# Kernel optimization log

Hardware: AMD Instinct MI355X
Metric: run time of the kernel (lower is better)

Reference implementation:

```python
import jax, jax.numpy as jnp
import numpy as np

N_NODES = 40000
N_EDGES = 640000
D_IN = 128
D_OUT = 128


def setup_inputs() -> dict:
    key = jax.random.key(0)
    k1, k2, k3 = jax.random.split(key, 3)
    x = jax.random.normal(k1, (N_NODES, D_IN), dtype=jnp.float32)
    W = jax.random.normal(k2, (D_IN, D_OUT), dtype=jnp.float32) / np.sqrt(D_IN)
    b = jnp.zeros((D_OUT,), dtype=jnp.float32)
    edge_index = jax.random.randint(k3, (2, N_EDGES), 0, N_NODES, dtype=jnp.int64)
    return {"x": x, "W": W, "b": b, "edge_index": edge_index}


def reference(x, W, b, edge_index):
    src, dst = edge_index[0], edge_index[1]
    n = x.shape[0]
    # asymmetric normalization: 1 / out-degree(src), inf -> 0
    deg = jax.ops.segment_sum(jnp.ones_like(src, dtype=x.dtype), src, num_segments=n)
    deg_inv = jnp.where(deg > 0, 1.0 / deg, 0.0)
    # GCNConv (add_self_loops=False, normalize=False): h = x @ W; msg_e = w_e * h[src_e]
    h = x @ W  # [N, D_OUT]
    msg = h[src] * deg_inv[src][:, None]  # [E, D_OUT] gather-weighted messages
    out = jax.ops.segment_sum(msg, dst, num_segments=n) + b  # scatter-add to dst
    return out
```

## Files before the change

kernel.cpp:

```cpp
#include <hip/hip_runtime.h>

#define N_NODES 40000
#define D 128
#define N_EDGES 640000
#define GRP 128
#define NKEY 313
#define TSIZE 2048
#define NTILE 313
#define GCAP 2560
#define NSLICE 32
#define SLICE_E 20000
#define SLICE_E4 5000
#define HALF_BINS 20000
#define HALF_W 10000
#define WROW 20000
#define SRCH_BLKS 64
#define GEMM_BLKS 625
#define XP 136

typedef __attribute__((ext_vector_type(8))) short short8_t;
typedef __attribute__((ext_vector_type(4))) float float4_t;

static __device__ __forceinline__ unsigned short f2bf(float f) {
  unsigned u = __float_as_uint(f);
  return (unsigned short)((u + 0x7fffu + ((u >> 16) & 1u)) >> 16);
}
static __device__ __forceinline__ float bf2f(unsigned short h) {
  return __uint_as_float(((unsigned)h) << 16);
}

static __device__ __forceinline__ void scan512(unsigned* s, int tid) {
  const int t2 = tid + 256;
#pragma unroll
  for (int off = 1; off < 512; off <<= 1) {
    unsigned a = (tid >= off) ? s[tid - off] : 0u;
    unsigned c = (t2 >= off) ? s[t2 - off] : 0u;
    __syncthreads();
    s[tid] += a;
    s[t2] += c;
    __syncthreads();
  }
}

__global__ __launch_bounds__(256) void k1(
    const float* __restrict__ x, const float* __restrict__ W,
    const int* __restrict__ src, const int* __restrict__ dst,
    unsigned* __restrict__ slabS, unsigned* __restrict__ slabP,
    unsigned* __restrict__ lofs, unsigned* __restrict__ epackT,
    unsigned short* __restrict__ hb) {
  __shared__ unsigned smem[12544];
  const int bid = blockIdx.x;
  const int tid = threadIdx.x;

  if (bid < SRCH_BLKS) {
    const int b = bid >> 1;
    const int h = bid & 1;
    for (int i = tid; i < HALF_W; i += 256) smem[i] = 0;
    __syncthreads();
    const int4* p4 = (const int4*)(src + b * SLICE_E);
    const unsigned lo = (unsigned)(h * HALF_BINS);
    for (int it = tid; it < SLICE_E4; it += 256) {
      const int4 v = p4[it];
      unsigned u;
      u = (unsigned)v.x - lo; if (u < HALF_BINS) atomicAdd(&smem[u >> 1], 1u << ((u & 1) * 16));
      u = (unsigned)v.y - lo; if (u < HALF_BINS) atomicAdd(&smem[u >> 1], 1u << ((u & 1) * 16));
      u = (unsigned)v.z - lo; if (u < HALF_BINS) atomicAdd(&smem[u >> 1], 1u << ((u & 1) * 16));
      u = (unsigned)v.w - lo; if (u < HALF_BINS) atomicAdd(&smem[u >> 1], 1u << ((u & 1) * 16));
    }
    __syncthreads();
    unsigned* row = slabS + (size_t)b * WROW + h * HALF_W;
    for (int i = tid; i < HALF_W; i += 256) row[i] = smem[i];
    return;
  }

  const int t = bid - SRCH_BLKS;
  if (t % 3 == 2) {
    const int cid = t / 3;
    unsigned* cnt = smem;
    unsigned* cur = smem + 320;
    unsigned* s = smem + 640;
    unsigned* buf = smem + 1152;
    const int t2 = tid + 256;
    if (tid < NKEY) cnt[tid] = 0;
    if (t2 < NKEY) cnt[t2] = 0;
    __syncthreads();

    const int e0 = cid * TSIZE;
    const int nE = (N_EDGES - e0) < TSIZE ? (N_EDGES - e0) : TSIZE;
    int4 sa, sb, da, db;
    const bool act = (tid * 8) < nE;
    if (act) {
      sa = *(const int4*)(src + e0 + tid * 8);
      sb = *(const int4*)(src + e0 + tid * 8 + 4);
      da = *(const int4*)(dst + e0 + tid * 8);
      db = *(const int4*)(dst + e0 + tid * 8 + 4);
      atomicAdd(&cnt[da.x >> 7], 1u);
      atomicAdd(&cnt[da.y >> 7], 1u);
      atomicAdd(&cnt[da.z >> 7], 1u);
      atomicAdd(&cnt[da.w >> 7], 1u);
      atomicAdd(&cnt[db.x >> 7], 1u);
      atomicAdd(&cnt[db.y >> 7], 1u);
      atomicAdd(&cnt[db.z >> 7], 1u);
      atomicAdd(&cnt[db.w >> 7], 1u);
    }
    __syncthreads();

    const unsigned v0 = (tid < NKEY) ? cnt[tid] : 0u;
    const unsigned v1 = (t2 < NKEY) ? cnt[t2] : 0u;
    s[tid] = v0;
    s[t2] = v1;
    __syncthreads();
    scan512(s, tid);
    if (tid < NKEY) {
      const unsigned ex = s[tid] - v0;
      cur[tid] = ex;
      slabP[(size_t)cid * NKEY + tid] = v0;
      lofs[(size_t)cid * NKEY + tid] = ex;
    }
    if (t2 < NKEY) {
      const unsigned ex = s[t2] - v1;
      cur[t2] = ex;
      slabP[(size_t)cid * NKEY + t2] = v1;
      lofs[(size_t)cid * NKEY + t2] = ex;
    }
    __syncthreads();

    if (act) {
#define TPLACE(DV, SV)                                                \
  {                                                                   \
    const int d_ = (DV);                                              \
    const unsigned r_ = atomicAdd(&cur[d_ >> 7], 1u);                 \
    buf[r_] = ((unsigned)(d_ & 127) << 16) | (unsigned)(SV);          \
  }
      TPLACE(da.x, sa.x) TPLACE(da.y, sa.y) TPLACE(da.z, sa.z) TPLACE(da.w, sa.w)
      TPLACE(db.x, sb.x) TPLACE(db.y, sb.y) TPLACE(db.z, sb.z) TPLACE(db.w, sb.w)
#undef TPLACE
    }
    __syncthreads();
    for (int i = tid; i < nE; i += 256) epackT[e0 + i] = buf[i];
    return;
  }

  const int gid = 2 * (t / 3) + (t % 3);
  if (gid >= GEMM_BLKS) return;
  const int n0 = gid * 64;
  const int w = tid >> 6;
  const int lane = tid & 63;

  unsigned short* wb = (unsigned short*)smem;
  unsigned short* xb = wb + 16384;

#pragma unroll 4
  for (int i = 0; i < 16; ++i) {
    const int g4 = i * 256 + tid;
    const int k = g4 >> 5;
    const int d0 = (g4 & 31) * 4;
    const float4 v = ((const float4*)W)[g4];
    const int q = k >> 5, r = k & 31;
    const int base =
        (((d0 >> 4) * 4 + q) * 64 + ((r >> 3) * 16 + (d0 & 15))) * 8 + (r & 7);
    wb[base] = f2bf(v.x);
    wb[base + 8] = f2bf(v.y);
    wb[base + 16] = f2bf(v.z);
    wb[base + 24] = f2bf(v.w);
  }

  {
    const float4* xg = (const float4*)(x + (size_t)n0 * D);
#pragma unroll
    for (int j = 0; j < 8; ++j) {
      const int idx = tid + j * 256;
      const int row = idx >> 5;
      const int c4 = idx & 31;
      const float4 v = xg[idx];
      ushort4 o;
      o.x = f2bf(v.x); o.y = f2bf(v.y); o.z = f2bf(v.z); o.w = f2bf(v.w);
      *(ushort4*)(xb + row * XP + c4 * 4) = o;
    }
  }
  __syncthreads();

  short8_t afrag[4];
  {
    const unsigned short* ap0 = xb + (w * 16 + (lane & 15)) * XP + (lane >> 4) * 8;
#pragma unroll
    for (int q = 0; q < 4; ++q) afrag[q] = *(const short8_t*)(ap0 + q * 32);
  }

  const int orow = n0 + w * 16 + (lane >> 4) * 4;
  const int ocolbase = lane & 15;
#pragma unroll
  for (int t8 = 0; t8 < 8; ++t8) {
    float4_t acc = {0.f, 0.f, 0.f, 0.f};
#pragma unroll
    for (int q = 0; q < 4; ++q) {
      const short8_t bfrag = *(const short8_t*)(wb + ((t8 * 4 + q) * 64 + lane) * 8);
      acc = __builtin_amdgcn_mfma_f32_16x16x32_bf16(afrag[q], bfrag, acc, 0, 0, 0);
    }
    const int col = t8 * 16 + ocolbase;
#pragma unroll
    for (int r = 0; r < 4; ++r)
      hb[(size_t)(orow + r) * D + col] = f2bf(acc[r]);
  }
}

__global__ __launch_bounds__(256) void k4a(
    const unsigned* __restrict__ slabP, const unsigned* __restrict__ lofs,
    const unsigned* __restrict__ epackT, const unsigned* __restrict__ slabS,
    int* __restrict__ offs, int* __restrict__ cnt_dst,
    unsigned short* __restrict__ esrc16, float* __restrict__ dinv) {
  const int bid = blockIdx.x;
  const int tid = threadIdx.x;

  if (bid < NKEY) {
    const int k = bid;
    __shared__ unsigned chb[NTILE];
    __shared__ unsigned chc[NTILE];
    __shared__ unsigned cnt[GRP];
    __shared__ unsigned cur[GRP];
    __shared__ unsigned s[256];

    for (int t = tid; t < NTILE; t += 256) {
      chc[t] = slabP[(size_t)t * NKEY + k];
      chb[t] = t * TSIZE + lofs[(size_t)t * NKEY + k];
    }
    if (tid < GRP) cnt[tid] = 0;
    __syncthreads();

    for (int t = tid; t < NTILE; t += 256) {
      const unsigned base = chb[t];
      const unsigned c = chc[t];
      for (unsigned e = 0; e < c; ++e) {
        atomicAdd(&cnt[epackT[base + e] >> 16], 1u);
      }
    }
    __syncthreads();

    const unsigned v = (tid < GRP) ? cnt[tid] : 0u;
    s[tid] = v;
    __syncthreads();
#pragma unroll
    for (int off = 1; off < 256; off <<= 1) {
      unsigned a = (tid >= off) ? s[tid - off] : 0u;
      __syncthreads();
      s[tid] += a;
      __syncthreads();
    }
    if (tid < GRP) {
      const unsigned ex = s[tid] - v;
      cur[tid] = ex;
      const int n = k * GRP + tid;
      if (n < N_NODES) {
        offs[n] = (int)(k * GCAP + ex);
        cnt_dst[n] = (int)v;
      }
    }
    __syncthreads();

    for (int t = tid; t < NTILE; t += 256) {
      const unsigned base = chb[t];
      const unsigned c = chc[t];
      for (unsigned e = 0; e < c; ++e) {
        const unsigned p = epackT[base + e];
        const unsigned r = atomicAdd(&cur[p >> 16], 1u);
        if (r < GCAP) esrc16[(size_t)k * GCAP + r] = (unsigned short)(p & 0xFFFFu);
      }
    }
    return;
  }

  const int w = (bid - NKEY) * 256 + tid;
  if (w >= WROW) return;
  unsigned run = 0;
#pragma unroll 8
  for (int b = 0; b < NSLICE; ++b) run += slabS[(size_t)b * WROW + w];
  const unsigned lo = run & 0xFFFFu;
  const unsigned hi = run >> 16;
  dinv[2 * w] = lo ? 1.0f / (float)lo : 0.0f;
  dinv[2 * w + 1] = hi ? 1.0f / (float)hi : 0.0f;
}

__global__ __launch_bounds__(256) void k4b(
    const int* __restrict__ offs, const int* __restrict__ cnt_dst,
    const float* __restrict__ dinv, const unsigned short* __restrict__ esrc16,
    const unsigned short* __restrict__ hb,
    const float* __restrict__ b, float* __restrict__ out) {
  const int tid = threadIdx.x;
  const int node = blockIdx.x * 8 + (tid >> 5);
  const int lane = tid & 31;

  const int start = offs[node];
  const int len = cnt_dst[node];
  const unsigned short* bk = esrc16 + start;

  int sj = 0;
  if (lane < len) sj = bk[lane];
  const float fj = dinv[sj];

  float4 aa[4];
#pragma unroll
  for (int q = 0; q < 4; ++q) aa[q] = make_float4(0.f, 0.f, 0.f, 0.f);

  const int l32 = len < 32 ? len : 32;
  for (int jj = 0; jj < l32; jj += 8) {
    ushort4 u[8];
    float fq[8];
#pragma unroll
    for (int q = 0; q < 8; ++q) {
      const int j = jj + q;
      const int s = __shfl(sj, j, 32);
      const float f = __shfl(fj, j, 32);
      const bool on = j < l32;
      const int ss = on ? s : 0;
      u[q] = ((const ushort4*)(hb + (size_t)ss * D))[lane];
      fq[q] = on ? f : 0.0f;
    }
#pragma unroll
    for (int q = 0; q < 8; ++q) {
      const float f = fq[q];
      float4& a = aa[q & 3];
      a.x += f * bf2f(u[q].x);
      a.y += f * bf2f(u[q].y);
      a.z += f * bf2f(u[q].z);
      a.w += f * bf2f(u[q].w);
    }
  }
  for (int j = 32; j < len; ++j) {
    const int s = bk[j];
    const float f = dinv[s];
    ushort4 u = ((const ushort4*)(hb + (size_t)s * D))[lane];
    aa[0].x += f * bf2f(u.x);
    aa[0].y += f * bf2f(u.y);
    aa[0].z += f * bf2f(u.z);
    aa[0].w += f * bf2f(u.w);
  }

  const float4 bias = ((const float4*)b)[lane];
  float4 v;
  v.x = bias.x + (aa[0].x + aa[1].x) + (aa[2].x + aa[3].x);
  v.y = bias.y + (aa[0].y + aa[1].y) + (aa[2].y + aa[3].y);
  v.z = bias.z + (aa[0].z + aa[1].z) + (aa[2].z + aa[3].z);
  v.w = bias.w + (aa[0].w + aa[1].w) + (aa[2].w + aa[3].w);
  ((float4*)(out + (size_t)node * D))[lane] = v;
}

extern "C" void kernel_launch(void* const* d_in, const int* in_sizes, int n_in,
                              void* d_out, int out_size, void* d_ws, size_t ws_size,
                              hipStream_t stream) {
  const float* x = (const float*)d_in[0];
  const float* W = (const float*)d_in[1];
  const float* b = (const float*)d_in[2];
  const int* ei = (const int*)d_in[3];
  const int* src = ei;
  const int* dst = ei + N_EDGES;
  float* out = (float*)d_out;

  char* ws = (char*)d_ws;
  float* dinv = (float*)(ws + 0);
  unsigned* slabS = (unsigned*)(ws + 160000);
  unsigned* slabP = (unsigned*)(ws + 2720000);
  unsigned* lofs = (unsigned*)(ws + 3112192);
  unsigned* epackT = (unsigned*)(ws + 3504384);
  int* offs = (int*)(ws + 6068480);
  int* cnt_dst = (int*)(ws + 6228480);
  unsigned short* esrc16 = (unsigned short*)(ws + 6388480);
  unsigned short* hb = (unsigned short*)(ws + 7991040);

  k1<<<SRCH_BLKS + 939, 256, 0, stream>>>(x, W, src, dst, slabS, slabP, lofs,
                                          epackT, hb);
  k4a<<<NKEY + 79, 256, 0, stream>>>(slabP, lofs, epackT, slabS, offs, cnt_dst,
                                     esrc16, dinv);
  k4b<<<5000, 256, 0, stream>>>(offs, cnt_dst, dinv, esrc16, hb, b, out);
}
```

Measured before the change: 71.11 us.

## Bucket edges directly into per-key global slots via atomic key cursors

Tile blocks now reserve space in a per-key global bucket with an atomicAdd on a key cursor and write packed edges straight into that bucket. They no longer write tile-local sorted chunks plus per-tile count and offset tables. The second kernel then reads each key's bucket contiguously instead of walking 313 small per-tile chunks with serial per-thread loops. This removes strided small-chunk reads and the slabP/lofs tables, at the cost of a memset, global atomics and scattered writes from the first kernel.

```diff
diff --git a/kernel.cpp b/kernel.cpp
--- a/kernel.cpp
+++ b/kernel.cpp
@@ -42,12 +42,11 @@
   }
 }
 
-__global__ __launch_bounds__(256) void k1(
+__global__ __launch_bounds__(256) void kA(
     const float* __restrict__ x, const float* __restrict__ W,
     const int* __restrict__ src, const int* __restrict__ dst,
-    unsigned* __restrict__ slabS, unsigned* __restrict__ slabP,
-    unsigned* __restrict__ lofs, unsigned* __restrict__ epackT,
-    unsigned short* __restrict__ hb) {
+    unsigned* __restrict__ slabS, unsigned* __restrict__ keycursor,
+    unsigned* __restrict__ epack, unsigned short* __restrict__ hb) {
   __shared__ unsigned smem[12544];
   const int bid = blockIdx.x;
   const int tid = threadIdx.x;
@@ -78,8 +77,9 @@
     const int cid = t / 3;
     unsigned* cnt = smem;
     unsigned* cur = smem + 320;
-    unsigned* s = smem + 640;
-    unsigned* buf = smem + 1152;
+    int* dlt = (int*)(smem + 640);
+    unsigned* s = smem + 960;
+    unsigned* buf = smem + 1536;
     const int t2 = tid + 256;
     if (tid < NKEY) cnt[tid] = 0;
     if (t2 < NKEY) cnt[t2] = 0;
@@ -114,30 +114,33 @@
     if (tid < NKEY) {
       const unsigned ex = s[tid] - v0;
       cur[tid] = ex;
-      slabP[(size_t)cid * NKEY + tid] = v0;
-      lofs[(size_t)cid * NKEY + tid] = ex;
+      if (v0 > 0) dlt[tid] = (int)atomicAdd(&keycursor[tid], v0) - (int)ex;
     }
     if (t2 < NKEY) {
       const unsigned ex = s[t2] - v1;
       cur[t2] = ex;
-      slabP[(size_t)cid * NKEY + t2] = v1;
-      lofs[(size_t)cid * NKEY + t2] = ex;
+      if (v1 > 0) dlt[t2] = (int)atomicAdd(&keycursor[t2], v1) - (int)ex;
     }
     __syncthreads();
 
     if (act) {
 #define TPLACE(DV, SV)                                                \
   {                                                                   \
-    const int d_ = (DV);                                              \
+    const unsigned d_ = (unsigned)(DV);                               \
     const unsigned r_ = atomicAdd(&cur[d_ >> 7], 1u);                 \
-    buf[r_] = ((unsigned)(d_ & 127) << 16) | (unsigned)(SV);          \
+    buf[r_] = (d_ << 16) | (unsigned)(SV);                            \
   }
       TPLACE(da.x, sa.x) TPLACE(da.y, sa.y) TPLACE(da.z, sa.z) TPLACE(da.w, sa.w)
       TPLACE(db.x, sb.x) TPLACE(db.y, sb.y) TPLACE(db.z, sb.z) TPLACE(db.w, sb.w)
 #undef TPLACE
     }
     __syncthreads();
-    for (int i = tid; i < nE; i += 256) epackT[e0 + i] = buf[i];
+    for (int i = tid; i < nE; i += 256) {
+      const unsigned p = buf[i];
+      const unsigned key = (p >> 16) >> 7;
+      const int off = i + dlt[key];
+      if (off < GCAP) epack[(size_t)key * GCAP + off] = p;
+    }
     return;
   }
 
@@ -204,35 +207,29 @@
   }
 }
 
-__global__ __launch_bounds__(256) void k4a(
-    const unsigned* __restrict__ slabP, const unsigned* __restrict__ lofs,
-    const unsigned* __restrict__ epackT, const unsigned* __restrict__ slabS,
-    int* __restrict__ offs, int* __restrict__ cnt_dst,
-    unsigned short* __restrict__ esrc16, float* __restrict__ dinv) {
+__global__ __launch_bounds__(256) void kB(
+    const unsigned* __restrict__ keycursor, const unsigned* __restrict__ epack,
+    const unsigned* __restrict__ slabS, int* __restrict__ offs,
+    int* __restrict__ cnt_dst, unsigned short* __restrict__ esrc16,
+    float* __restrict__ dinv) {
   const int bid = blockIdx.x;
   const int tid = threadIdx.x;
 
   if (bid < NKEY) {
     const int k = bid;
-    __shared__ unsigned chb[NTILE];
-    __shared__ unsigned chc[NTILE];
     __shared__ unsigned cnt[GRP];
     __shared__ unsigned cur[GRP];
     __shared__ unsigned s[256];
 
-    for (int t = tid; t < NTILE; t += 256) {
-      chc[t] = slabP[(size_t)t * NKEY + k];
-      chb[t] = t * TSIZE + lofs[(size_t)t * NKEY + k];
-    }
+    unsigned used = keycursor[k];
+    if (used > GCAP) used = GCAP;
+    const size_t base = (size_t)k * GCAP;
+
     if (tid < GRP) cnt[tid] = 0;
     __syncthreads();
 
-    for (int t = tid; t < NTILE; t += 256) {
-      const unsigned base = chb[t];
-      const unsigned c = chc[t];
-      for (unsigned e = 0; e < c; ++e) {
-        atomicAdd(&cnt[epackT[base + e] >> 16], 1u);
-      }
+    for (unsigned i = tid; i < used; i += 256) {
+      atomicAdd(&cnt[(epack[base + i] >> 16) & 127], 1u);
     }
     __syncthreads();
 
@@ -251,20 +248,17 @@
       cur[tid] = ex;
       const int n = k * GRP + tid;
       if (n < N_NODES) {
-        offs[n] = (int)(k * GCAP + ex);
+        offs[n] = (int)(base + ex);
         cnt_dst[n] = (int)v;
       }
     }
     __syncthreads();
 
-    for (int t = tid; t < NTILE; t += 256) {
-      const unsigned base = chb[t];
-      const unsigned c = chc[t];
-      for (unsigned e = 0; e < c; ++e) {
-        const unsigned p = epackT[base + e];
-        const unsigned r = atomicAdd(&cur[p >> 16], 1u);
-        if (r < GCAP) esrc16[(size_t)k * GCAP + r] = (unsigned short)(p & 0xFFFFu);
-      }
+    for (unsigned i = tid; i < used; i += 256) {
+      const unsigned p = epack[base + i];
+      const unsigned dl = (p >> 16) & 127;
+      const unsigned r = atomicAdd(&cur[dl], 1u);
+      esrc16[base + r] = (unsigned short)(p & 0xFFFFu);
     }
     return;
   }
@@ -358,17 +352,17 @@
   char* ws = (char*)d_ws;
   float* dinv = (float*)(ws + 0);
   unsigned* slabS = (unsigned*)(ws + 160000);
-  unsigned* slabP = (unsigned*)(ws + 2720000);
-  unsigned* lofs = (unsigned*)(ws + 3112192);
-  unsigned* epackT = (unsigned*)(ws + 3504384);
-  int* offs = (int*)(ws + 6068480);
-  int* cnt_dst = (int*)(ws + 6228480);
-  unsigned short* esrc16 = (unsigned short*)(ws + 6388480);
-  unsigned short* hb = (unsigned short*)(ws + 7991040);
-
-  k1<<<SRCH_BLKS + 939, 256, 0, stream>>>(x, W, src, dst, slabS, slabP, lofs,
-                                          epackT, hb);
-  k4a<<<NKEY + 79, 256, 0, stream>>>(slabP, lofs, epackT, slabS, offs, cnt_dst,
-                                     esrc16, dinv);
+  unsigned* keycursor = (unsigned*)(ws + 2720000);
+  unsigned* epack = (unsigned*)(ws + 2724096);
+  int* offs = (int*)(ws + 5929216);
+  int* cnt_dst = (int*)(ws + 6089216);
+  unsigned short* esrc16 = (unsigned short*)(ws + 6249216);
+  unsigned short* hb = (unsigned short*)(ws + 7851776);
+
+  hipMemsetAsync(keycursor, 0, NKEY * 4, stream);
+  kA<<<SRCH_BLKS + 939, 256, 0, stream>>>(x, W, src, dst, slabS, keycursor,
+                                          epack, hb);
+  kB<<<NKEY + 79, 256, 0, stream>>>(keycursor, epack, slabS, offs, cnt_dst,
+                                    esrc16, dinv);
   k4b<<<5000, 256, 0, stream>>>(offs, cnt_dst, dinv, esrc16, hb, b, out);
 }
```

New measurement: 63.05 us. 11.3% less time.
